# Kernel tuning notes

Measured on AMD Instinct MI355X. Metric: run time of the kernel, lower is better.

The kernel has to match this reference:

```python
import jax, jax.numpy as jnp
import numpy as np

N = 50000      # nodes
E = 800000     # edges (before self-loops)
F_IN = 512     # input features
H = 8          # heads (layer 1)
C = 32         # hidden per head
CLS = 40       # classes


def setup_inputs() -> dict:
    key = jax.random.key(0)
    ks = jax.random.split(key, 10)
    small = lambda k, shape: jax.random.normal(k, shape, jnp.float32) * 0.05
    return {
        "x": jax.random.normal(ks[0], (N, F_IN), jnp.float32),
        "edge_index": jax.random.randint(ks[1], (2, E), 0, N, jnp.int32),
        # layer 1 params (GATConv: F_IN -> C per head, 8 heads, concat)
        "W1": small(ks[2], (F_IN, H * C)),
        "a_src1": small(ks[3], (H, C)),
        "a_dst1": small(ks[4], (H, C)),
        "b1": jnp.zeros((H * C,), jnp.float32),
        # layer 2 params (GATConv: H*C -> CLS, 1 head)
        "W2": small(ks[5], (H * C, CLS)),
        "a_src2": small(ks[6], (1, CLS)),
        "a_dst2": small(ks[7], (1, CLS)),
        "b2": jnp.zeros((CLS,), jnp.float32),
    }


def gat_conv(x, W, a_src, a_dst, b, src, dst, n):
    """PyG-style GATConv (negative_slope=0.2); self-loops already in src/dst."""
    h_, c_ = a_src.shape
    h = (x @ W).reshape(n, h_, c_)                       # [N, H, C]
    alpha_src = jnp.einsum('nhc,hc->nh', h, a_src)       # [N, H]
    alpha_dst = jnp.einsum('nhc,hc->nh', h, a_dst)       # [N, H]
    e = jax.nn.leaky_relu(alpha_src[src] + alpha_dst[dst], 0.2)  # [E', H]
    # segment softmax over incoming edges of each destination node
    m = jax.lax.stop_gradient(jax.ops.segment_max(e, dst, num_segments=n))
    ex = jnp.exp(e - m[dst])
    den = jax.ops.segment_sum(ex, dst, num_segments=n)
    alpha = ex / (den[dst] + 1e-16)                      # [E', H]
    out = jax.ops.segment_sum(h[src] * alpha[:, :, None], dst, num_segments=n)
    return out.reshape(n, h_ * c_) + b


def reference(x, edge_index, W1, a_src1, a_dst1, b1, W2, a_src2, a_dst2, b2):
    n = x.shape[0]
    loop = jnp.arange(n, dtype=edge_index.dtype)
    src = jnp.concatenate([edge_index[0], loop])  # add self-loops (PyG default)
    dst = jnp.concatenate([edge_index[1], loop])
    # dropout is identity at inference
    h = jax.nn.elu(gat_conv(x, W1, a_src1, a_dst1, b1, src, dst, n))
    out = gat_conv(h, W2, a_src2, a_dst2, b2, src, dst, n)
    return jax.nn.log_softmax(out, axis=1)
```

## Files before the change

kernel.cpp:

```cpp
#include <hip/hip_runtime.h>
#include <hip/hip_bf16.h>
#include <math.h>

constexpr int NN  = 50000;
constexpr int NE  = 800000;
constexpr int EP  = NE + NN;
constexpr int FIN = 512;
constexpr int NH  = 8;
constexpr int NC  = 32;
constexpr int HC  = NH * NC;
constexpr int CLS = 40;
constexpr int CLSP = 48;
constexpr int NGB = (NN + 63) / 64;
constexpr int NSB = 1024;

typedef __attribute__((ext_vector_type(8))) __bf16 bf16x8;
typedef __attribute__((ext_vector_type(4))) __bf16 bf16x4;
typedef __attribute__((ext_vector_type(4))) float f32x4;
typedef __attribute__((ext_vector_type(2))) float f32x2;

__device__ inline bf16x8 cvt8(const float4 a, const float4 b) {
  bf16x8 o;
  o[0] = (__bf16)a.x; o[1] = (__bf16)a.y; o[2] = (__bf16)a.z; o[3] = (__bf16)a.w;
  o[4] = (__bf16)b.x; o[5] = (__bf16)b.y; o[6] = (__bf16)b.z; o[7] = (__bf16)b.w;
  return o;
}

__device__ inline unsigned char to_fp8(float f) {
  int pk = __builtin_amdgcn_cvt_pk_fp8_f32(f, f, 0, false);
  return (unsigned char)(pk & 0xff);
}

__global__ void k_hist(const int* __restrict__ ei, int* __restrict__ deg) {
  int e = blockIdx.x * 256 + threadIdx.x;
  if (e >= EP) return;
  int d = (e < NE) ? ei[NE + e] : (e - NE);
  atomicAdd(&deg[d], 1);
}

__global__ __launch_bounds__(1024) void k_scan1(const int* __restrict__ deg,
                                                int* __restrict__ rowptr1,
                                                int* __restrict__ bsum, int n) {
  __shared__ int sm[1024];
  int i = blockIdx.x * 1024 + threadIdx.x;
  int v = (i < n) ? deg[i] : 0;
  sm[threadIdx.x] = v;
  __syncthreads();
  for (int off = 1; off < 1024; off <<= 1) {
    int t = (threadIdx.x >= off) ? sm[threadIdx.x - off] : 0;
    __syncthreads();
    sm[threadIdx.x] += t;
    __syncthreads();
  }
  if (i < n) rowptr1[i] = sm[threadIdx.x];
  if (threadIdx.x == 1023) bsum[blockIdx.x] = sm[1023];
}

__global__ void k_scan2(int* __restrict__ bsum, int nb) {
  int lane = threadIdx.x;
  int v = (lane < nb) ? bsum[lane] : 0;
#pragma unroll
  for (int off = 1; off < 64; off <<= 1) {
    int t = __shfl_up(v, off);
    if (lane >= off) v += t;
  }
  int ex = __shfl_up(v, 1);
  if (lane == 0) ex = 0;
  if (lane < nb) bsum[lane] = ex;
}

__global__ void k_scan3(int* __restrict__ rowptr, const int* __restrict__ bsum,
                        int* __restrict__ cursor, int n) {
  int i = blockIdx.x * 256 + threadIdx.x;
  if (i == 0) { rowptr[0] = 0; cursor[0] = 0; }
  if (i < n) {
    int v = rowptr[i + 1] + bsum[i >> 10];
    rowptr[i + 1] = v;
    if (i + 1 < n) cursor[i + 1] = v;
  }
}

__global__ void k_cvt_w(const float* __restrict__ W1, const float* __restrict__ W2,
                        __bf16* __restrict__ Wt, __bf16* __restrict__ W2t) {
  int t = blockIdx.x * 256 + threadIdx.x;
  if (t < HC * (FIN / 8)) {
    int c = t >> 6, kq = (t & 63) * 8;
    bf16x8 o;
#pragma unroll
    for (int j = 0; j < 8; ++j) o[j] = (__bf16)W1[(size_t)(kq + j) * HC + c];
    *(bf16x8*)&Wt[(size_t)c * FIN + kq] = o;
  } else {
    int u = t - HC * (FIN / 8);
    if (u < CLSP * HC) {
      int c = u >> 8, k = u & 255;
      W2t[u] = (c < CLS) ? (__bf16)W2[(size_t)k * CLS + c] : (__bf16)0.f;
    }
  }
}

__global__ __launch_bounds__(256, 4) void k_gemm1_scatter(
    const float* __restrict__ X, const __bf16* __restrict__ Wt,
    const float* __restrict__ a_s1, const float* __restrict__ a_d1,
    unsigned char* __restrict__ Hout, float* __restrict__ asrc1,
    float* __restrict__ adst1,
    const int* __restrict__ ei, int* __restrict__ cursor,
    int* __restrict__ srcS) {
  __shared__ __align__(16) __bf16 As[64 * 8 * 8];
  const int tid = threadIdx.x;

  if (blockIdx.x >= NGB) {
    int base = (blockIdx.x - NGB) * 256 + tid;
    for (int e = base; e < EP; e += NSB * 256) {
      int s, d;
      if (e < NE) { s = ei[e]; d = ei[NE + e]; } else { s = d = e - NE; }
      int p = atomicAdd(&cursor[d], 1);
      srcS[p] = s;
    }
    return;
  }

  const int lane = tid & 63;
  const int w    = tid >> 6;
  const int wn   = w * 64;
  const int bm   = blockIdx.x * 64;

  const int ar   = tid >> 2;
  const int ak   = (tid & 3) * 16;
  const int kb0  = ak >> 3;
  const int asw  = ar & 7;
  const int arow = min(bm + ar, NN - 1);
  const int l15  = lane & 15, lg = lane >> 4;

  f32x4 acc[4][4] = {};

#pragma unroll
  for (int k0 = 0; k0 < FIN; k0 += 64) {
    {
      const float* gx = &X[(size_t)arow * FIN + k0 + ak];
      float4 f0 = *(const float4*)(gx + 0);
      float4 f1 = *(const float4*)(gx + 4);
      float4 f2 = *(const float4*)(gx + 8);
      float4 f3 = *(const float4*)(gx + 12);
      *(bf16x8*)(As + (size_t)(ar * 8 + (kb0 ^ asw)) * 8)       = cvt8(f0, f1);
      *(bf16x8*)(As + (size_t)(ar * 8 + ((kb0 + 1) ^ asw)) * 8) = cvt8(f2, f3);
    }
    __syncthreads();

#pragma unroll
    for (int kh = 0; kh < 2; ++kh) {
      const int kb = lg + 4 * kh;
      bf16x8 bv[4];
#pragma unroll
      for (int ni = 0; ni < 4; ++ni)
        bv[ni] = *(const bf16x8*)(Wt + (size_t)(wn + ni * 16 + l15) * FIN + k0 + kb * 8);
#pragma unroll
      for (int mi = 0; mi < 4; ++mi) {
        int r = mi * 16 + l15;
        bf16x8 av = *(const bf16x8*)(As + (size_t)(r * 8 + (kb ^ (r & 7))) * 8);
#pragma unroll
        for (int ni = 0; ni < 4; ++ni)
          acc[mi][ni] = __builtin_amdgcn_mfma_f32_16x16x32_bf16(
              av, bv[ni], acc[mi][ni], 0, 0, 0);
      }
    }
    __syncthreads();
  }

  const int hbase = 2 * w;
#pragma unroll
  for (int hh = 0; hh < 2; ++hh) {
    float asA = a_s1[(hbase + hh) * NC + l15];
    float asB = a_s1[(hbase + hh) * NC + 16 + l15];
    float adA = a_d1[(hbase + hh) * NC + l15];
    float adB = a_d1[(hbase + hh) * NC + 16 + l15];
    float vs = 0.f, vd = 0.f;
#pragma unroll
    for (int mi = 0; mi < 4; ++mi) {
#pragma unroll
      for (int r = 0; r < 4; ++r) {
        float ps = acc[mi][2 * hh][r] * asA + acc[mi][2 * hh + 1][r] * asB;
        float pd = acc[mi][2 * hh][r] * adA + acc[mi][2 * hh + 1][r] * adB;
#pragma unroll
        for (int off = 1; off < 16; off <<= 1) {
          ps += __shfl_xor(ps, off, 64);
          pd += __shfl_xor(pd, off, 64);
        }
        if (l15 == mi * 4 + r) { vs = ps; vd = pd; }
      }
    }
    int rw = bm + (l15 >> 2) * 16 + lg * 4 + (l15 & 3);
    if (rw < NN) {
      asrc1[(size_t)rw * NH + hbase + hh] = vs;
      adst1[(size_t)rw * NH + hbase + hh] = vd;
    }
  }

#pragma unroll
  for (int mi = 0; mi < 4; ++mi) {
#pragma unroll
    for (int ni = 0; ni < 4; ++ni) {
      int col = wn + ni * 16 + l15;
#pragma unroll
      for (int r = 0; r < 4; ++r) {
        int row = bm + mi * 16 + lg * 4 + r;
        if (row < NN) Hout[(size_t)row * HC + col] = to_fp8(acc[mi][ni][r]);
      }
    }
  }
}

__global__ __launch_bounds__(256) void k_agg1(const unsigned char* __restrict__ h1f8,
                                              const float* __restrict__ asrc,
                                              const float* __restrict__ adst,
                                              const int* __restrict__ srcS,
                                              const int* __restrict__ rowptr,
                                              const float* __restrict__ b1,
                                              __bf16* __restrict__ helu) {
  int wave = (blockIdx.x * 256 + threadIdx.x) >> 6;
  int lane = threadIdx.x & 63;
  if (wave >= NN) return;
  int lo = rowptr[wave], hi = rowptr[wave + 1];
  int head = lane >> 3;
  int hw   = lane & 7;
  float adstv = adst[wave * NH + head];
  float ad2   = adst[wave * NH + hw];
  float4 acc = {0.f, 0.f, 0.f, 0.f};
  float den = 0.f;

  for (int base = lo; base < hi; base += 64) {
    int cnt = hi - base; if (cnt > 64) cnt = 64;
    int sv = (lane < cnt) ? srcS[base + lane] : 0;
    int j = 0;
    for (; j + 8 <= cnt; j += 8) {
      int se = __shfl(sv, j + head);
      float v = asrc[se * NH + hw] + ad2;
      v = v > 0.f ? v : 0.2f * v;
      float wv = __expf(v);
      int s[8]; unsigned int hv[8];
#pragma unroll
      for (int u = 0; u < 8; ++u) s[u] = __shfl(sv, j + u);
#pragma unroll
      for (int u = 0; u < 8; ++u)
        hv[u] = *(const unsigned int*)&h1f8[(size_t)s[u] * HC + lane * 4];
#pragma unroll
      for (int u = 0; u < 8; ++u) {
        float wu = __shfl(wv, u * 8 + head);
        f32x2 lo2 = __builtin_amdgcn_cvt_pk_f32_fp8(hv[u], false);
        f32x2 hi2 = __builtin_amdgcn_cvt_pk_f32_fp8(hv[u], true);
        acc.x += wu * lo2.x;
        acc.y += wu * lo2.y;
        acc.z += wu * hi2.x;
        acc.w += wu * hi2.y;
        den += wu;
      }
    }
    for (; j < cnt; ++j) {
      int s = __shfl(sv, j);
      float v = asrc[s * NH + head] + adstv;
      v = v > 0.f ? v : 0.2f * v;
      float w = __expf(v);
      unsigned int hv = *(const unsigned int*)&h1f8[(size_t)s * HC + lane * 4];
      f32x2 lo2 = __builtin_amdgcn_cvt_pk_f32_fp8(hv, false);
      f32x2 hi2 = __builtin_amdgcn_cvt_pk_f32_fp8(hv, true);
      acc.x += w * lo2.x;
      acc.y += w * lo2.y;
      acc.z += w * hi2.x;
      acc.w += w * hi2.y;
      den += w;
    }
  }

  float inv = 1.f / (den + 1e-16f);
  float4 bb = *(const float4*)&b1[lane * 4];
  float o[4] = {acc.x * inv + bb.x, acc.y * inv + bb.y,
                acc.z * inv + bb.z, acc.w * inv + bb.w};
  bf16x4 ov;
#pragma unroll
  for (int j2 = 0; j2 < 4; ++j2) {
    float e = o[j2] > 0.f ? o[j2] : expm1f(o[j2]);
    ov[j2] = (__bf16)e;
  }
  *(bf16x4*)&helu[(size_t)wave * HC + lane * 4] = ov;
}

__global__ __launch_bounds__(256) void k_gemm2m(const __bf16* __restrict__ A,
                                                const __bf16* __restrict__ W2t,
                                                const float* __restrict__ a_s2,
                                                const float* __restrict__ a_d2,
                                                __bf16* __restrict__ Hout,
                                                float* __restrict__ asrc2,
                                                float* __restrict__ adst2) {
  __shared__ __align__(16) __bf16 As[128 * 8 * 8];
  __shared__ __align__(16) __bf16 Bsh[CLSP * 33 * 8];
  const int tid  = threadIdx.x;
  const int lane = tid & 63;
  const int w    = tid >> 6;
  const int wm   = w * 32;
  const int bm   = blockIdx.x * 128;

  const int l3 = lane >> 3;
  const int l7 = lane & 7;
  const int kb_src = l7 ^ l3;

  for (int s = tid; s < CLSP * 32; s += 256) {
    int c = s >> 5, kb = s & 31;
    *(bf16x8*)(Bsh + (size_t)(c * 33 + kb) * 8) =
        *(const bf16x8*)(W2t + (size_t)c * HC + kb * 8);
  }

  f32x4 acc[2][3] = {};

  for (int step = 0; step < 4; ++step) {
    const int k0 = step * 64;
#pragma unroll
    for (int q = 0; q < 4; ++q) {
      const int inst = w * 4 + q;
      const int r = inst * 8 + l3;
      const int arow = min(bm + r, NN - 1);
      const __bf16* ga = A + (size_t)arow * HC + k0 + kb_src * 8;
      __builtin_amdgcn_global_load_lds(
          (const __attribute__((address_space(1))) void*)ga,
          (__attribute__((address_space(3))) void*)(As + inst * 512), 16, 0, 0);
    }
    __syncthreads();

    const int l15 = lane & 15, lg = lane >> 4;
#pragma unroll
    for (int kh = 0; kh < 2; ++kh) {
      const int kbl = lg + 4 * kh;
      const int kbg = step * 8 + kbl;
      bf16x8 av[2], bv[3];
#pragma unroll
      for (int mi = 0; mi < 2; ++mi) {
        int r = wm + mi * 16 + l15;
        av[mi] = *(const bf16x8*)(As + (size_t)(r * 8 + (kbl ^ (r & 7))) * 8);
      }
#pragma unroll
      for (int ni = 0; ni < 3; ++ni) {
        int c = ni * 16 + l15;
        bv[ni] = *(const bf16x8*)(Bsh + (size_t)(c * 33 + kbg) * 8);
      }
#pragma unroll
      for (int mi = 0; mi < 2; ++mi)
#pragma unroll
        for (int ni = 0; ni < 3; ++ni)
          acc[mi][ni] = __builtin_amdgcn_mfma_f32_16x16x32_bf16(
              av[mi], bv[ni], acc[mi][ni], 0, 0, 0);
    }
    __syncthreads();
  }

  const int l15 = lane & 15, lg = lane >> 4;

  {
    int c0 = l15, c1 = 16 + l15, c2 = 32 + l15;
    float as0 = a_s2[c0], as1 = a_s2[c1], as2v = (c2 < CLS) ? a_s2[c2] : 0.f;
    float ad0 = a_d2[c0], ad1 = a_d2[c1], ad2v = (c2 < CLS) ? a_d2[c2] : 0.f;
    float vs = 0.f, vd = 0.f;
#pragma unroll
    for (int mi = 0; mi < 2; ++mi) {
#pragma unroll
      for (int r = 0; r < 4; ++r) {
        float ps = acc[mi][0][r] * as0 + acc[mi][1][r] * as1 + acc[mi][2][r] * as2v;
        float pd = acc[mi][0][r] * ad0 + acc[mi][1][r] * ad1 + acc[mi][2][r] * ad2v;
#pragma unroll
        for (int off = 1; off < 16; off <<= 1) {
          ps += __shfl_xor(ps, off, 64);
          pd += __shfl_xor(pd, off, 64);
        }
        if (l15 == mi * 4 + r) { vs = ps; vd = pd; }
      }
    }
    int rw = bm + wm + (l15 >> 2) * 16 + lg * 4 + (l15 & 3);
    if (l15 < 8 && rw < NN) {
      asrc2[rw] = vs;
      adst2[rw] = vd;
    }
  }

#pragma unroll
  for (int mi = 0; mi < 2; ++mi) {
#pragma unroll
    for (int ni = 0; ni < 3; ++ni) {
      int col = ni * 16 + l15;
      if (col >= CLS) continue;
#pragma unroll
      for (int r = 0; r < 4; ++r) {
        int row = bm + wm + mi * 16 + lg * 4 + r;
        if (row < NN) Hout[(size_t)row * CLS + col] = (__bf16)acc[mi][ni][r];
      }
    }
  }
}

__global__ __launch_bounds__(256) void k_agg2(const __bf16* __restrict__ h2b,
                                              const float* __restrict__ asrc,
                                              const float* __restrict__ adst,
                                              const int* __restrict__ srcS,
                                              const int* __restrict__ rowptr,
                                              const float* __restrict__ b2,
                                              float* __restrict__ out) {
  int wave = (blockIdx.x * 256 + threadIdx.x) >> 6;
  int lane = threadIdx.x & 63;
  if (wave >= NN) return;
  int lo = rowptr[wave], hi = rowptr[wave + 1];
  bool act = lane < CLS;
  float adstv = adst[wave];
  float acc = 0.f, den = 0.f;

  for (int base = lo; base < hi; base += 64) {
    int cnt = hi - base; if (cnt > 64) cnt = 64;
    int sv = (lane < cnt) ? srcS[base + lane] : 0;
    float v = asrc[sv] + adstv;
    v = v > 0.f ? v : 0.2f * v;
    float wv = __expf(v);
    int j = 0;
    for (; j + 8 <= cnt; j += 8) {
      int s[8]; float hval[8];
#pragma unroll
      for (int u = 0; u < 8; ++u) s[u] = __shfl(sv, j + u);
#pragma unroll
      for (int u = 0; u < 8; ++u)
        hval[u] = act ? (float)h2b[(size_t)s[u] * CLS + lane] : 0.f;
#pragma unroll
      for (int u = 0; u < 8; ++u) {
        float wu = __shfl(wv, j + u);
        acc += wu * hval[u];
        den += wu;
      }
    }
    for (; j < cnt; ++j) {
      int s = __shfl(sv, j);
      float wu = __shfl(wv, j);
      if (act) acc += wu * (float)h2b[(size_t)s * CLS + lane];
      den += wu;
    }
  }

  float o = act ? (acc / (den + 1e-16f) + b2[lane]) : -INFINITY;
  float m = o;
#pragma unroll
  for (int off = 32; off; off >>= 1) m = fmaxf(m, __shfl_xor(m, off, 64));
  float ex = act ? __expf(o - m) : 0.f;
  float ssum = ex;
#pragma unroll
  for (int off = 32; off; off >>= 1) ssum += __shfl_xor(ssum, off, 64);
  if (act) out[(size_t)wave * CLS + lane] = o - m - logf(ssum);
}

extern "C" void kernel_launch(void* const* d_in, const int* in_sizes, int n_in,
                              void* d_out, int out_size, void* d_ws, size_t ws_size,
                              hipStream_t stream) {
  const float* x      = (const float*)d_in[0];
  const int*   ei     = (const int*)d_in[1];
  const float* W1     = (const float*)d_in[2];
  const float* a_src1 = (const float*)d_in[3];
  const float* a_dst1 = (const float*)d_in[4];
  const float* b1     = (const float*)d_in[5];
  const float* W2     = (const float*)d_in[6];
  const float* a_src2 = (const float*)d_in[7];
  const float* a_dst2 = (const float*)d_in[8];
  const float* b2     = (const float*)d_in[9];
  float* out = (float*)d_out;

  char* p = (char*)d_ws;
  auto alloc = [&](size_t bytes) {
    char* r = p;
    p += (bytes + 255) & ~size_t(255);
    return r;
  };
  unsigned char* h1f8 = (unsigned char*)alloc((size_t)NN * HC);
  __bf16* helu  = (__bf16*)alloc((size_t)NN * HC * 2);
  __bf16* Wt    = (__bf16*)alloc((size_t)HC * FIN * 2);
  __bf16* W2t   = (__bf16*)alloc((size_t)CLSP * HC * 2);
  __bf16* h2b   = (__bf16*)alloc((size_t)NN * CLS * 2);
  float*  asrc1 = (float*)alloc((size_t)NN * NH * 4);
  float*  adst1 = (float*)alloc((size_t)NN * NH * 4);
  float*  asrc2 = (float*)alloc((size_t)NN * 4);
  float*  adst2 = (float*)alloc((size_t)NN * 4);
  int*    srcS  = (int*)alloc((size_t)EP * 4);
  int*    deg   = (int*)alloc((size_t)NN * 4);
  int*    cursor= (int*)alloc((size_t)NN * 4);
  int*    rowptr= (int*)alloc((size_t)(NN + 1) * 4);
  int*    bsum  = (int*)alloc(256 * 4);

  hipMemsetAsync(deg, 0, (size_t)NN * 4, stream);

  const int nbScan = (NN + 1023) / 1024;
  k_hist<<<(EP + 255) / 256, 256, 0, stream>>>(ei, deg);
  k_scan1<<<nbScan, 1024, 0, stream>>>(deg, rowptr + 1, bsum, NN);
  k_scan2<<<1, 64, 0, stream>>>(bsum, nbScan);
  k_scan3<<<(NN + 255) / 256, 256, 0, stream>>>(rowptr, bsum, cursor, NN);

  k_cvt_w<<<(HC * (FIN / 8) + CLSP * HC + 255) / 256, 256, 0, stream>>>(W1, W2, Wt, W2t);

  k_gemm1_scatter<<<NGB + NSB, 256, 0, stream>>>(x, Wt, a_src1, a_dst1,
                                                 h1f8, asrc1, adst1,
                                                 ei, cursor, srcS);

  k_agg1<<<(NN + 3) / 4, 256, 0, stream>>>(h1f8, asrc1, adst1, srcS, rowptr, b1, helu);

  k_gemm2m<<<(NN + 127) / 128, 256, 0, stream>>>(helu, W2t, a_src2, a_dst2,
                                                 h2b, asrc2, adst2);
  k_agg2<<<(NN + 3) / 4, 256, 0, stream>>>(h2b, asrc2, adst2, srcS, rowptr, b2, out);
}
```

Baseline: 228.9 us.

## Double-buffer X tiles via direct global-to-LDS loads and shrink CSR indices to 16-bit

```diff
diff --git a/kernel.cpp b/kernel.cpp
--- a/kernel.cpp
+++ b/kernel.cpp
@@ -20,6 +20,13 @@
 typedef __attribute__((ext_vector_type(2))) float f32x2;
 
 __device__ inline bf16x8 cvt8(const float4 a, const float4 b) {
+  bf16x8 o;
+  o[0] = (__bf16)a.x; o[1] = (__bf16)a.y; o[2] = (__bf16)a.z; o[3] = (__bf16)a.w;
+  o[4] = (__bf16)b.x; o[5] = (__bf16)b.y; o[6] = (__bf16)b.z; o[7] = (__bf16)b.w;
+  return o;
+}
+
+__device__ inline bf16x8 cvt8v(const f32x4 a, const f32x4 b) {
   bf16x8 o;
   o[0] = (__bf16)a.x; o[1] = (__bf16)a.y; o[2] = (__bf16)a.z; o[3] = (__bf16)a.w;
   o[4] = (__bf16)b.x; o[5] = (__bf16)b.y; o[6] = (__bf16)b.z; o[7] = (__bf16)b.w;
@@ -98,14 +105,14 @@
   }
 }
 
-__global__ __launch_bounds__(256, 4) void k_gemm1_scatter(
+__global__ __launch_bounds__(256) void k_gemm1_scatter(
     const float* __restrict__ X, const __bf16* __restrict__ Wt,
     const float* __restrict__ a_s1, const float* __restrict__ a_d1,
     unsigned char* __restrict__ Hout, float* __restrict__ asrc1,
     float* __restrict__ adst1,
     const int* __restrict__ ei, int* __restrict__ cursor,
-    int* __restrict__ srcS) {
-  __shared__ __align__(16) __bf16 As[64 * 8 * 8];
+    unsigned short* __restrict__ srcS) {
+  __shared__ __align__(16) float Xp[2][4096];
   const int tid = threadIdx.x;
 
   if (blockIdx.x >= NGB) {
@@ -114,7 +121,7 @@
       int s, d;
       if (e < NE) { s = ei[e]; d = ei[NE + e]; } else { s = d = e - NE; }
       int p = atomicAdd(&cursor[d], 1);
-      srcS[p] = s;
+      srcS[p] = (unsigned short)s;
     }
     return;
   }
@@ -123,28 +130,33 @@
   const int w    = tid >> 6;
   const int wn   = w * 64;
   const int bm   = blockIdx.x * 64;
-
-  const int ar   = tid >> 2;
-  const int ak   = (tid & 3) * 16;
-  const int kb0  = ak >> 3;
-  const int asw  = ar & 7;
-  const int arow = min(bm + ar, NN - 1);
   const int l15  = lane & 15, lg = lane >> 4;
 
+  const int srow_l  = (lane >> 4);
+  const int sslot   = (l15 >> 1);
+  const int shalf   = (lane & 1);
+
   f32x4 acc[4][4] = {};
 
-#pragma unroll
-  for (int k0 = 0; k0 < FIN; k0 += 64) {
-    {
-      const float* gx = &X[(size_t)arow * FIN + k0 + ak];
-      float4 f0 = *(const float4*)(gx + 0);
-      float4 f1 = *(const float4*)(gx + 4);
-      float4 f2 = *(const float4*)(gx + 8);
-      float4 f3 = *(const float4*)(gx + 12);
-      *(bf16x8*)(As + (size_t)(ar * 8 + (kb0 ^ asw)) * 8)       = cvt8(f0, f1);
-      *(bf16x8*)(As + (size_t)(ar * 8 + ((kb0 + 1) ^ asw)) * 8) = cvt8(f2, f3);
-    }
+  auto issue = [&](int c, int buf) {
+#pragma unroll
+    for (int jj = 0; jj < 4; ++jj) {
+      const int j = w * 4 + jj;
+      const int row_l = 4 * j + srow_l;
+      const int rowG = min(bm + row_l, NN - 1);
+      const int g = sslot ^ (row_l & 7);
+      const float* src = X + (size_t)rowG * FIN + c * 64 + g * 8 + shalf * 4;
+      __builtin_amdgcn_global_load_lds(
+          (const __attribute__((address_space(1))) void*)src,
+          (__attribute__((address_space(3))) void*)(&Xp[buf][j * 256]), 16, 0, 0);
+    }
+  };
+
+  issue(0, 0);
+  for (int c = 0; c < 8; ++c) {
+    const int cur = c & 1;
     __syncthreads();
+    if (c < 7) issue(c + 1, cur ^ 1);
 
 #pragma unroll
     for (int kh = 0; kh < 2; ++kh) {
@@ -152,11 +164,15 @@
       bf16x8 bv[4];
 #pragma unroll
       for (int ni = 0; ni < 4; ++ni)
-        bv[ni] = *(const bf16x8*)(Wt + (size_t)(wn + ni * 16 + l15) * FIN + k0 + kb * 8);
+        bv[ni] = *(const bf16x8*)(Wt + (size_t)(wn + ni * 16 + l15) * FIN
+                                     + c * 64 + kb * 8);
 #pragma unroll
       for (int mi = 0; mi < 4; ++mi) {
         int r = mi * 16 + l15;
-        bf16x8 av = *(const bf16x8*)(As + (size_t)(r * 8 + (kb ^ (r & 7))) * 8);
+        int fo = r * 64 + ((kb ^ (r & 7)) << 3);
+        f32x4 alo = *(const f32x4*)&Xp[cur][fo];
+        f32x4 ahi = *(const f32x4*)&Xp[cur][fo + 4];
+        bf16x8 av = cvt8v(alo, ahi);
 #pragma unroll
         for (int ni = 0; ni < 4; ++ni)
           acc[mi][ni] = __builtin_amdgcn_mfma_f32_16x16x32_bf16(
@@ -212,7 +228,7 @@
 __global__ __launch_bounds__(256) void k_agg1(const unsigned char* __restrict__ h1f8,
                                               const float* __restrict__ asrc,
                                               const float* __restrict__ adst,
-                                              const int* __restrict__ srcS,
+                                              const unsigned short* __restrict__ srcS,
                                               const int* __restrict__ rowptr,
                                               const float* __restrict__ b1,
                                               __bf16* __restrict__ helu) {
@@ -229,7 +245,7 @@
 
   for (int base = lo; base < hi; base += 64) {
     int cnt = hi - base; if (cnt > 64) cnt = 64;
-    int sv = (lane < cnt) ? srcS[base + lane] : 0;
+    int sv = (lane < cnt) ? (int)srcS[base + lane] : 0;
     int j = 0;
     for (; j + 8 <= cnt; j += 8) {
       int se = __shfl(sv, j + head);
@@ -396,7 +412,7 @@
 __global__ __launch_bounds__(256) void k_agg2(const __bf16* __restrict__ h2b,
                                               const float* __restrict__ asrc,
                                               const float* __restrict__ adst,
-                                              const int* __restrict__ srcS,
+                                              const unsigned short* __restrict__ srcS,
                                               const int* __restrict__ rowptr,
                                               const float* __restrict__ b2,
                                               float* __restrict__ out) {
@@ -410,7 +426,7 @@
 
   for (int base = lo; base < hi; base += 64) {
     int cnt = hi - base; if (cnt > 64) cnt = 64;
-    int sv = (lane < cnt) ? srcS[base + lane] : 0;
+    int sv = (lane < cnt) ? (int)srcS[base + lane] : 0;
     float v = asrc[sv] + adstv;
     v = v > 0.f ? v : 0.2f * v;
     float wv = __expf(v);
@@ -478,7 +494,7 @@
   float*  adst1 = (float*)alloc((size_t)NN * NH * 4);
   float*  asrc2 = (float*)alloc((size_t)NN * 4);
   float*  adst2 = (float*)alloc((size_t)NN * 4);
-  int*    srcS  = (int*)alloc((size_t)EP * 4);
+  unsigned short* srcS = (unsigned short*)alloc((size_t)EP * 2);
   int*    deg   = (int*)alloc((size_t)NN * 4);
   int*    cursor= (int*)alloc((size_t)NN * 4);
   int*    rowptr= (int*)alloc((size_t)(NN + 1) * 4);
```

New measurement: 231.6 us. No clear change (+1.2%).
